# Kernel tuning notes

Hardware: AMD Instinct MI355X
Metric: run time of the kernel (lower is better)

## Reference

```python
import jax, jax.numpy as jnp
import numpy as np

EPS = 1e-5  # PyTorch BatchNorm1d default eps


def _bn_relu(x, gamma, beta):
    # BatchNorm1d in training mode: batch statistics (biased variance), then ReLU
    mu = x.mean(0, keepdims=True)
    var = ((x - mu) ** 2).mean(0, keepdims=True)
    return jax.nn.relu(gamma * (x - mu) / jnp.sqrt(var + EPS) + beta)


def _conv_t(x, w, b, stride, pad):
    # ConvTranspose1d. x: [B,Cin,L]; w: [Cin,Cout,K] (torch layout).
    # Implemented as lhs-dilated conv with flipped kernel; out_len = (L-1)*stride - 2*pad + K
    k = w.shape[-1]
    wk = jnp.transpose(jnp.flip(w, -1), (1, 0, 2))  # [Cout,Cin,K]
    y = jax.lax.conv_general_dilated(
        x, wk, window_strides=(1,), padding=[(k - 1 - pad, k - 1 - pad)],
        lhs_dilation=(stride,), dimension_numbers=("NCH", "OIH", "NCH"))
    return y + b[None, :, None]


def _lorentz(S):
    # Vectorized form of the original triple loop over (batch i, freq j, triad k).
    # S: [B, L], L % 3 == 0. Triads (wp, w0, g) = S[:, k], S[:, k+1], S[:, k+2].
    B, L = S.shape
    w = (0.8 + jnp.arange(L, dtype=S.dtype) / L)[None, :, None]  # [1,L,1] frequency grid
    wp2 = (S[:, 0::3] ** 2)[:, None, :]  # [B,1,K]
    w0 = S[:, 1::3][:, None, :]
    g = S[:, 2::3][:, None, :]
    sub1 = w0 ** 2 - w ** 2                      # [B,L,K]
    denom = sub1 ** 2 + (w * g) ** 2
    e1 = wp2 * sub1 / denom
    e2 = wp2 * w * g / denom
    m = 0.5 * (e1 ** 2 + e2 ** 2)
    n = jnp.sqrt(jnp.maximum(m + 0.5 * e1, 0.0))   # clamp guards sqrt(neg) -> NaN
    kap2 = jnp.maximum(m - 0.5 * e1, 0.0)          # kappa^2 (original squares it anyway)
    dT = 4.0 * n / ((n + 1.0) ** 2 + kap2)
    return dT.sum(-1)  # reduce over triads -> [B,L]


def setup_inputs() -> dict:
    key = jax.random.key(0)
    ks = iter(jax.random.split(key, 40))
    B = 2048
    dims = [8, 1024, 1024, 150]
    d = {"G": jax.random.normal(next(ks), (B, dims[0]), jnp.float32)}
    for i in range(3):
        fi, fo = dims[i], dims[i + 1]
        d[f"w{i+1}"] = jax.random.normal(next(ks), (fo, fi), jnp.float32) / float(np.sqrt(fi))
        d[f"b{i+1}"] = jnp.zeros((fo,), jnp.float32)
        d[f"g{i+1}"] = 1.0 + 0.1 * jax.random.normal(next(ks), (fo,), jnp.float32)
        d[f"be{i+1}"] = 0.1 * jax.random.normal(next(ks), (fo,), jnp.float32)
    specs = [(1, 4, 8), (4, 4, 5), (4, 4, 5)]  # (in_ch, out_ch, kernel)
    for i, (ci, co, k) in enumerate(specs):
        d[f"ct{i+1}_w"] = jax.random.normal(next(ks), (ci, co, k), jnp.float32) / float(np.sqrt(ci * k))
        d[f"ct{i+1}_b"] = 0.01 * jax.random.normal(next(ks), (co,), jnp.float32)
    d["cf_w"] = jax.random.normal(next(ks), (1, 4, 1), jnp.float32) / 2.0
    d["cf_b"] = 0.01 * jax.random.normal(next(ks), (1,), jnp.float32)
    return d


def reference(G, w1, b1, g1, be1, w2, b2, g2, be2, w3, b3, g3, be3,
              ct1_w, ct1_b, ct2_w, ct2_b, ct3_w, ct3_b, cf_w, cf_b):
    out = _bn_relu(G @ w1.T + b1, g1, be1)
    out = _bn_relu(out @ w2.T + b2, g2, be2)
    out = _bn_relu(out @ w3.T + b3, g3, be3)
    out = out[:, None, :]                       # [B,1,150]
    out = _conv_t(out, ct1_w, ct1_b, 2, 3)      # [B,4,300]
    out = _conv_t(out, ct2_w, ct2_b, 1, 2)      # [B,4,300]
    out = _conv_t(out, ct3_w, ct3_b, 1, 2)      # [B,4,300]
    out = jax.lax.conv_general_dilated(
        out, cf_w, (1,), [(0, 0)], dimension_numbers=("NCH", "OIH", "NCH")) + cf_b[None, :, None]
    S = out[:, 0, :]                            # squeeze -> [B,300]
    return _lorentz(S)
```

## Files before the change

kernel.cpp:

```cpp
#include <hip/hip_runtime.h>
#include <hip/hip_bf16.h>

#define EPS 1e-5f

typedef __attribute__((ext_vector_type(8))) short bf16x8;
typedef __attribute__((ext_vector_type(4))) float f32x4;

__device__ __forceinline__ void gload16(const void* g, void* l) {
  __builtin_amdgcn_global_load_lds(
      (const __attribute__((address_space(1))) unsigned int*)g,
      (__attribute__((address_space(3))) unsigned int*)l, 16, 0, 0);
}

__device__ __forceinline__ void split2(float x, short& h, short& l) {
  unsigned u = __float_as_uint(x);
  h = (short)(u >> 16);
  float hf = __uint_as_float(u & 0xFFFF0000u);
  l = (short)(__float_as_uint(x - hf) >> 16);
}
__device__ __forceinline__ void bn_coef(float s, float q, float g, float be,
                                        float& sc, float& sh) {
  float mu = s * (1.f / 2048.f);
  float var = q * (1.f / 2048.f) - mu * mu;
  sc = g * rsqrtf(var + EPS);
  sh = be - mu * sc;
}

__global__ __launch_bounds__(256) void kpre(
    const float* __restrict__ W2, const float* __restrict__ W3,
    ushort* __restrict__ W2thi, ushort* __restrict__ W2tlo,
    ushort* __restrict__ W3hi, ushort* __restrict__ W3lo,
    float4* __restrict__ stv, float4* __restrict__ Y3v,
    float4* __restrict__ outv) {
  int b = blockIdx.x;
  int tid = threadIdx.x;
  if (b < 1024) {
    int c = tid * 4;
    int nt = b >> 6, rr = b & 63;
    int kt = c >> 6, chunk = (c >> 3) & 7, e = c & 7;
    float4 v = *(const float4*)&W2[(size_t)b * 1024 + c];
    float ev[4] = {v.x, v.y, v.z, v.w};
    short hh[4], ll[4];
#pragma unroll
    for (int q = 0; q < 4; ++q) split2(ev[q], hh[q], ll[q]);
    size_t o = ((size_t)(nt * 16 + kt) << 12) + rr * 64 + ((chunk ^ (rr & 7)) << 3) + e;
    *(ushort4*)&W2thi[o] = make_ushort4((ushort)hh[0], (ushort)hh[1],
                                        (ushort)hh[2], (ushort)hh[3]);
    *(ushort4*)&W2tlo[o] = make_ushort4((ushort)ll[0], (ushort)ll[1],
                                        (ushort)ll[2], (ushort)ll[3]);
  } else if (b < 1029) {
    int idx = (b - 1024) * 256 + tid;
    if (idx < 1112) stv[idx] = make_float4(0.f, 0.f, 0.f, 0.f);
  } else if (b < 1189) {
    int n = b - 1029;
    int c = tid * 4;
    float4 v = make_float4(0.f, 0.f, 0.f, 0.f);
    if (n < 150) v = *(const float4*)&W3[(size_t)n * 1024 + c];
    float e[4] = {v.x, v.y, v.z, v.w};
    short hh[4], ll[4];
#pragma unroll
    for (int q = 0; q < 4; ++q) split2(e[q], hh[q], ll[q]);
    *(ushort4*)&W3hi[(size_t)n * 1024 + c] =
        make_ushort4((ushort)hh[0], (ushort)hh[1], (ushort)hh[2], (ushort)hh[3]);
    *(ushort4*)&W3lo[(size_t)n * 1024 + c] =
        make_ushort4((ushort)ll[0], (ushort)ll[1], (ushort)ll[2], (ushort)ll[3]);
  } else if (b < 1489) {
    Y3v[(b - 1189) * 256 + tid] = make_float4(0.f, 0.f, 0.f, 0.f);
  } else {
    outv[(b - 1489) * 256 + tid] = make_float4(0.f, 0.f, 0.f, 0.f);
  }
}

__global__ __launch_bounds__(256) void k1s(const float* __restrict__ G,
                                           const float* __restrict__ W1,
                                           float* __restrict__ sA1,
                                           float* __restrict__ qA1) {
  int r0 = blockIdx.x * 8;
  int c = threadIdx.x * 4;
  float w[4][8];
#pragma unroll
  for (int q = 0; q < 4; ++q)
#pragma unroll
    for (int k = 0; k < 8; ++k) w[q][k] = W1[(c + q) * 8 + k];
  float s[4] = {}, ss[4] = {};
  for (int r = 0; r < 8; ++r) {
    const float4 g0 = *(const float4*)&G[(size_t)(r0 + r) * 8];
    const float4 g1 = *(const float4*)&G[(size_t)(r0 + r) * 8 + 4];
    float gr[8] = {g0.x, g0.y, g0.z, g0.w, g1.x, g1.y, g1.z, g1.w};
#pragma unroll
    for (int q = 0; q < 4; ++q) {
      float acc = 0.f;
#pragma unroll
      for (int k = 0; k < 8; ++k) acc += gr[k] * w[q][k];
      s[q] += acc;
      ss[q] += acc * acc;
    }
  }
#pragma unroll
  for (int q = 0; q < 4; ++q) {
    atomicAdd(&sA1[c + q], s[q]);
    atomicAdd(&qA1[c + q], ss[q]);
  }
}

__global__ __launch_bounds__(256) void k1c(
    const float* __restrict__ G, const float* __restrict__ W1,
    const float* __restrict__ sA1, const float* __restrict__ qA1,
    const float* __restrict__ g1, const float* __restrict__ be1,
    ushort* __restrict__ X1thi, ushort* __restrict__ X1tlo) {
  int r0 = blockIdx.x * 8;
  int c = threadIdx.x * 4;
  float w[4][8];
#pragma unroll
  for (int q = 0; q < 4; ++q)
#pragma unroll
    for (int k = 0; k < 8; ++k) w[q][k] = W1[(c + q) * 8 + k];
  float sc[4], sh[4];
#pragma unroll
  for (int q = 0; q < 4; ++q)
    bn_coef(sA1[c + q], qA1[c + q], g1[c + q], be1[c + q], sc[q], sh[q]);
  int kt = c >> 6, chunk = (c >> 3) & 7, e = c & 7;
  for (int r = 0; r < 8; ++r) {
    int b = r0 + r;
    const float4 g0 = *(const float4*)&G[(size_t)b * 8];
    const float4 g1v = *(const float4*)&G[(size_t)b * 8 + 4];
    float gr[8] = {g0.x, g0.y, g0.z, g0.w, g1v.x, g1v.y, g1v.z, g1v.w};
    short hs[4], ls[4];
#pragma unroll
    for (int q = 0; q < 4; ++q) {
      float acc = 0.f;
#pragma unroll
      for (int k = 0; k < 8; ++k) acc += gr[k] * w[q][k];
      float x = fmaxf(0.f, acc * sc[q] + sh[q]);
      split2(x, hs[q], ls[q]);
    }
    int mt = b >> 7, rr = b & 127;
    size_t o = ((size_t)(mt * 16 + kt) << 13) + rr * 64 + ((chunk ^ (rr & 7)) << 3) + e;
    *(ushort4*)&X1thi[o] = make_ushort4((ushort)hs[0], (ushort)hs[1],
                                        (ushort)hs[2], (ushort)hs[3]);
    *(ushort4*)&X1tlo[o] = make_ushort4((ushort)ls[0], (ushort)ls[1],
                                        (ushort)ls[2], (ushort)ls[3]);
  }
}

__global__ __launch_bounds__(512) void k2_mfma(
    const ushort* __restrict__ X1thi, const ushort* __restrict__ X1tlo,
    const ushort* __restrict__ W2thi, const ushort* __restrict__ W2tlo,
    float* __restrict__ Y2, float* __restrict__ sA2, float* __restrict__ qA2) {
  __shared__ short lAhi[128 * 64], lAlo[128 * 64];
  __shared__ short lBhi[64 * 64], lBlo[64 * 64];
  int id = blockIdx.x;
  int xcd = id & 7, slot = id >> 3;
  int g = slot >> 4, wi = slot & 15;
  int bx = (xcd & 3) * 4 + (wi & 3);
  int by = ((xcd >> 2) * 2 + g) * 4 + (wi >> 2);
  int b0 = bx * 128, j0 = by * 64;
  int tid = threadIdx.x;
  int lane = tid & 63, wave = tid >> 6;
  int wm = wave >> 1, wn = wave & 1;
  int woff = wave * 1024 + lane * 16;
  int loff = wave * 1024;
  f32x4 acc[2][2] = {};
  for (int kt = 0; kt < 16; ++kt) {
    const char* ga = (const char*)(X1thi + ((size_t)(bx * 16 + kt) << 13));
    const char* gl = (const char*)(X1tlo + ((size_t)(bx * 16 + kt) << 13));
    const char* gb = (const char*)(W2thi + ((size_t)(by * 16 + kt) << 12));
    const char* gc = (const char*)(W2tlo + ((size_t)(by * 16 + kt) << 12));
    gload16(ga + woff, (char*)lAhi + loff);
    gload16(ga + woff + 8192, (char*)lAhi + loff + 8192);
    gload16(gl + woff, (char*)lAlo + loff);
    gload16(gl + woff + 8192, (char*)lAlo + loff + 8192);
    gload16(gb + woff, (char*)lBhi + loff);
    gload16(gc + woff, (char*)lBlo + loff);
    __syncthreads();
#pragma unroll
    for (int kk = 0; kk < 2; ++kk) {
      int ch = kk * 4 + (lane >> 4);
      bf16x8 ah[2], al[2], bh[2], bl[2];
#pragma unroll
      for (int mi = 0; mi < 2; ++mi) {
        int rr = wm * 32 + mi * 16 + (lane & 15);
        int ad = rr * 64 + ((ch ^ (rr & 7)) << 3);
        ah[mi] = *(const bf16x8*)&lAhi[ad];
        al[mi] = *(const bf16x8*)&lAlo[ad];
      }
#pragma unroll
      for (int ni = 0; ni < 2; ++ni) {
        int rr = wn * 32 + ni * 16 + (lane & 15);
        int bd = rr * 64 + ((ch ^ (rr & 7)) << 3);
        bh[ni] = *(const bf16x8*)&lBhi[bd];
        bl[ni] = *(const bf16x8*)&lBlo[bd];
      }
#pragma unroll
      for (int mi = 0; mi < 2; ++mi)
#pragma unroll
        for (int ni = 0; ni < 2; ++ni) {
          acc[mi][ni] = __builtin_amdgcn_mfma_f32_16x16x32_bf16(
              ah[mi], bh[ni], acc[mi][ni], 0, 0, 0);
          acc[mi][ni] = __builtin_amdgcn_mfma_f32_16x16x32_bf16(
              al[mi], bh[ni], acc[mi][ni], 0, 0, 0);
          acc[mi][ni] = __builtin_amdgcn_mfma_f32_16x16x32_bf16(
              ah[mi], bl[ni], acc[mi][ni], 0, 0, 0);
        }
    }
    __syncthreads();
  }
#pragma unroll
  for (int mi = 0; mi < 2; ++mi)
#pragma unroll
    for (int ni = 0; ni < 2; ++ni) {
      int col = j0 + wn * 32 + ni * 16 + (lane & 15);
#pragma unroll
      for (int r = 0; r < 4; ++r) {
        int row = b0 + wm * 32 + mi * 16 + (lane >> 4) * 4 + r;
        Y2[(size_t)row * 1024 + col] = acc[mi][ni][r];
      }
    }
#pragma unroll
  for (int ni = 0; ni < 2; ++ni) {
    float s = 0.f, q = 0.f;
#pragma unroll
    for (int mi = 0; mi < 2; ++mi)
#pragma unroll
      for (int r = 0; r < 4; ++r) {
        float v = acc[mi][ni][r];
        s += v;
        q += v * v;
      }
    s += __shfl_xor(s, 16);
    q += __shfl_xor(q, 16);
    s += __shfl_xor(s, 32);
    q += __shfl_xor(q, 32);
    if ((lane >> 4) == 0) {
      int col = j0 + wn * 32 + ni * 16 + lane;
      atomicAdd(&sA2[col], s);
      atomicAdd(&qA2[col], q);
    }
  }
}

__global__ __launch_bounds__(256) void k4_mfma(
    const float* __restrict__ Y2, const float* __restrict__ sA2,
    const float* __restrict__ qA2, const float* __restrict__ g2,
    const float* __restrict__ be2, const ushort* __restrict__ W3hi,
    const ushort* __restrict__ W3lo, float* __restrict__ Y3) {
  __shared__ short lAhi[32 * 64], lAlo[32 * 64];
  int b0 = blockIdx.x * 32;
  int kb = blockIdx.y * 128;
  int tid = threadIdx.x;
  int lane = tid & 63, wave = tid >> 6;
  int wm = wave & 1, wn = wave >> 1;
  f32x4 acc[5] = {};
  int srow = tid >> 3, sch = tid & 7;
  for (int k0 = 0; k0 < 128; k0 += 64) {
    int kg = kb + k0 + sch * 8;
    const float* src = &Y2[(size_t)(b0 + srow) * 1024 + kg];
    float4 f0 = *(const float4*)src;
    float4 f1 = *(const float4*)(src + 4);
    float4 sv0 = *(const float4*)&sA2[kg];
    float4 sv1 = *(const float4*)&sA2[kg + 4];
    float4 qv0 = *(const float4*)&qA2[kg];
    float4 qv1 = *(const float4*)&qA2[kg + 4];
    float4 gv0 = *(const float4*)&g2[kg];
    float4 gv1 = *(const float4*)&g2[kg + 4];
    float4 bv0 = *(const float4*)&be2[kg];
    float4 bv1 = *(const float4*)&be2[kg + 4];
    float e[8] = {f0.x, f0.y, f0.z, f0.w, f1.x, f1.y, f1.z, f1.w};
    float sv[8] = {sv0.x, sv0.y, sv0.z, sv0.w, sv1.x, sv1.y, sv1.z, sv1.w};
    float qv[8] = {qv0.x, qv0.y, qv0.z, qv0.w, qv1.x, qv1.y, qv1.z, qv1.w};
    float gv[8] = {gv0.x, gv0.y, gv0.z, gv0.w, gv1.x, gv1.y, gv1.z, gv1.w};
    float bev[8] = {bv0.x, bv0.y, bv0.z, bv0.w, bv1.x, bv1.y, bv1.z, bv1.w};
    bf16x8 hh, ll;
#pragma unroll
    for (int q = 0; q < 8; ++q) {
      float sc, sh;
      bn_coef(sv[q], qv[q], gv[q], bev[q], sc, sh);
      float x = fmaxf(0.f, fmaf(e[q], sc, sh));
      short h, l;
      split2(x, h, l);
      hh[q] = h;
      ll[q] = l;
    }
    if (k0) __syncthreads();
    int d = srow * 64 + ((sch ^ (srow & 7)) << 3);
    *(bf16x8*)&lAhi[d] = hh;
    *(bf16x8*)&lAlo[d] = ll;
    __syncthreads();
#pragma unroll
    for (int kk = 0; kk < 2; ++kk) {
      int r = wm * 16 + (lane & 15);
      int ch = kk * 4 + (lane >> 4);
      int ad = r * 64 + ((ch ^ (r & 7)) << 3);
      bf16x8 ah = *(const bf16x8*)&lAhi[ad];
      bf16x8 al = *(const bf16x8*)&lAlo[ad];
#pragma unroll
      for (int ni = 0; ni < 5; ++ni) {
        int col = wn * 80 + ni * 16 + (lane & 15);
        size_t wo = (size_t)col * 1024 + kb + k0 + kk * 32 + (lane >> 4) * 8;
        bf16x8 bh = *(const bf16x8*)&W3hi[wo];
        bf16x8 bl = *(const bf16x8*)&W3lo[wo];
        acc[ni] = __builtin_amdgcn_mfma_f32_16x16x32_bf16(ah, bh, acc[ni], 0, 0, 0);
        acc[ni] = __builtin_amdgcn_mfma_f32_16x16x32_bf16(al, bh, acc[ni], 0, 0, 0);
        acc[ni] = __builtin_amdgcn_mfma_f32_16x16x32_bf16(ah, bl, acc[ni], 0, 0, 0);
      }
    }
  }
#pragma unroll
  for (int ni = 0; ni < 5; ++ni) {
    int col = wn * 80 + ni * 16 + (lane & 15);
    if (col < 150) {
#pragma unroll
      for (int r = 0; r < 4; ++r) {
        int row = b0 + wm * 16 + (lane >> 4) * 4 + r;
        atomicAdd(&Y3[(size_t)row * 150 + col], acc[ni][r]);
      }
    }
  }
}

__global__ __launch_bounds__(256) void k5s(const float* __restrict__ Y3,
                                           float* __restrict__ sA3,
                                           float* __restrict__ qA3) {
  int r0 = blockIdx.x * 8;
  int j = threadIdx.x;
  if (j >= 150) return;
  float s = 0.f, q = 0.f;
  for (int r = 0; r < 8; ++r) {
    float v = Y3[(size_t)(r0 + r) * 150 + j];
    s += v;
    q += v * v;
  }
  atomicAdd(&sA3[j], s);
  atomicAdd(&qA3[j], q);
}

__global__ __launch_bounds__(256) void k6a(
    const float* __restrict__ Y3, const float* __restrict__ sA3,
    const float* __restrict__ qA3, const float* __restrict__ g3,
    const float* __restrict__ be3, const float* __restrict__ ct1_w,
    const float* __restrict__ ct1_b, const float* __restrict__ ct2_w,
    const float* __restrict__ ct2_b, const float* __restrict__ ct3_w,
    const float* __restrict__ ct3_b, const float* __restrict__ cf_w,
    const float* __restrict__ cf_b, float* __restrict__ Spre) {
  __shared__ float wt1[32], wb1[4], wt2L[80], wb2L[4], w3fL[20];
  __shared__ float Cc[36], cfb2C[1], cfbraw[1];
  __shared__ float h0p[4][160];
  __shared__ float hA[4][4][312];
  __shared__ float Srow[4][304];
  int tid = threadIdx.x;
  if (tid < 32) wt1[tid] = ct1_w[tid];
  else if (tid < 36) wb1[tid - 32] = ct1_b[tid - 32];
  else if (tid < 116) wt2L[tid - 36] = ct2_w[tid - 36];
  else if (tid < 120) wb2L[tid - 116] = ct2_b[tid - 116];
  else if (tid < 140) {
    int i = (tid - 120) / 5, j = (tid - 120) % 5;
    float s = 0.f;
#pragma unroll
    for (int p = 0; p < 4; ++p) s += cf_w[p] * ct3_w[(i * 4 + p) * 5 + j];
    w3fL[tid - 120] = s;
  } else if (tid == 140) {
    float s = cf_b[0];
#pragma unroll
    for (int p = 0; p < 4; ++p) s += cf_w[p] * ct3_b[p];
    cfbraw[0] = s;
  }
  int w = tid >> 6;
  int lane = tid & 63;
  int r = blockIdx.x * 4 + w;
  for (int i = lane; i < 160; i += 64) {
    int k = i - 2;
    float v = 0.f;
    if (k >= 0 && k < 150) {
      float sc, sh;
      bn_coef(sA3[k], qA3[k], g3[k], be3[k], sc, sh);
      v = fmaxf(0.f, Y3[(size_t)r * 150 + k] * sc + sh);
    }
    h0p[w][i] = v;
  }
  if (lane < 12) {
    int z = (lane < 4) ? lane : (300 + lane);
#pragma unroll
    for (int o = 0; o < 4; ++o) hA[w][o][z] = 0.f;
  }
  __syncthreads();
  if (tid < 36) {
    int i = tid / 9, u = tid % 9;
    float s = 0.f;
#pragma unroll
    for (int o = 0; o < 4; ++o) {
      int j2lo = (u > 4) ? (u - 4) : 0;
      int j2hi = (u < 4) ? u : 4;
      for (int j2 = j2lo; j2 <= j2hi; ++j2)
        s += wt2L[(i * 4 + o) * 5 + (u - j2)] * w3fL[o * 5 + j2];
    }
    Cc[tid] = s;
  } else if (tid == 36) {
    float s = cfbraw[0];
#pragma unroll
    for (int o = 0; o < 4; ++o) {
      float t = 0.f;
#pragma unroll
      for (int j2 = 0; j2 < 5; ++j2) t += w3fL[o * 5 + j2];
      s += wb2L[o] * t;
    }
    cfb2C[0] = s;
  }
  __syncthreads();
  for (int t = lane; t < 300; t += 64) {
    int p1 = (t + 3) & 1;
    int base = (t + 3 - p1) >> 1;
    float x0 = h0p[w][2 + base];
    float x1 = h0p[w][1 + base];
    float x2 = h0p[w][base];
    float x3 = h0p[w][base - 1];
#pragma unroll
    for (int o = 0; o < 4; ++o) {
      float acc = wb1[o];
      acc += wt1[o * 8 + p1] * x0;
      acc += wt1[o * 8 + p1 + 2] * x1;
      acc += wt1[o * 8 + p1 + 4] * x2;
      acc += wt1[o * 8 + p1 + 6] * x3;
      hA[w][o][4 + t] = acc;
    }
  }
  __syncthreads();
  for (int t = lane; t < 300; t += 64) {
    float acc = cfb2C[0];
#pragma unroll
    for (int i = 0; i < 4; ++i)
#pragma unroll
      for (int u = 0; u < 9; ++u) acc += Cc[i * 9 + u] * hA[w][i][t + 8 - u];
    if (t < 2) {
      for (int j2 = t + 3; j2 <= 4; ++j2) {
        int tp_ = t + 2 - j2;
        float corr = 0.f;
        for (int o = 0; o < 4; ++o) {
          float hb = wb2L[o];
          for (int i2 = 0; i2 < 4; ++i2)
            for (int j1 = 0; j1 < 5; ++j1)
              hb += wt2L[(i2 * 4 + o) * 5 + j1] * hA[w][i2][6 + tp_ - j1];
          corr += w3fL[o * 5 + j2] * hb;
        }
        acc -= corr;
      }
    }
    if (t > 297) {
      for (int j2 = 0; j2 <= t - 298; ++j2) {
        int tp_ = t + 2 - j2;
        float corr = 0.f;
        for (int o = 0; o < 4; ++o) {
          float hb = wb2L[o];
          for (int i2 = 0; i2 < 4; ++i2)
            for (int j1 = 0; j1 < 5; ++j1)
              hb += wt2L[(i2 * 4 + o) * 5 + j1] * hA[w][i2][6 + tp_ - j1];
          corr += w3fL[o * 5 + j2] * hb;
        }
        acc -= corr;
      }
    }
    Srow[w][t] = acc;
  }
  __syncthreads();
  for (int cc = lane; cc < 100; cc += 64) {
    float s0 = Srow[w][3 * cc], s1 = Srow[w][3 * cc + 1], s2 = Srow[w][3 * cc + 2];
    float P = s0 * s0, s1s = s1 * s1, s2s = s2 * s2;
    float halfP = 0.5f * P;
    float4 q0, q1;
    q0.x = s2s - 2.f * s1s;
    q0.y = s1s * s1s;
    q0.z = halfP * (P + s1s);
    q0.w = halfP;
    q1.x = halfP * (P - s1s);
    q1.y = 0.f;
    q1.z = 0.f;
    q1.w = 0.f;
    size_t o = ((size_t)r * 100 + cc) * 8;
    *(float4*)&Spre[o] = q0;
    *(float4*)&Spre[o + 4] = q1;
  }
}

__global__ __launch_bounds__(320) void k6b(const float* __restrict__ Spre,
                                           float* __restrict__ out) {
  int b = blockIdx.x;
  int l = threadIdx.x;
  float wl = 0.8f + (float)l * (1.0f / 300.0f);
  float x = wl * wl;
  float xn = -x;
  float acc = 0.f;
  const float4* pp = (const float4*)(Spre + (size_t)b * 800) + blockIdx.y * 50;
#pragma unroll 5
  for (int cc = 0; cc < 25; ++cc) {
    float4 q0 = pp[2 * cc];
    float4 q1 = pp[2 * cc + 1];
    float D = fmaf(x, x + q0.x, q0.y);
    float t1 = fmaxf(fmaf(q0.w, xn, q0.z), 0.f);
    float t2 = fmaxf(fmaf(q0.w, x, q1.x), 0.f);
    float R = __builtin_amdgcn_sqrtf(t1 * D);
    float sum = (t1 + D) + fmaf(2.f, R, t2);
    acc = fmaf(R, __builtin_amdgcn_rcpf(sum), acc);
  }
  if (l < 300) atomicAdd(&out[(size_t)b * 300 + l], 4.0f * acc);
}

extern "C" void kernel_launch(void* const* d_in, const int* in_sizes, int n_in,
                              void* d_out, int out_size, void* d_ws,
                              size_t ws_size, hipStream_t stream) {
  const float* G = (const float*)d_in[0];
  const float* w1 = (const float*)d_in[1];
  const float* g1 = (const float*)d_in[3];
  const float* be1 = (const float*)d_in[4];
  const float* w2 = (const float*)d_in[5];
  const float* g2 = (const float*)d_in[7];
  const float* be2 = (const float*)d_in[8];
  const float* w3 = (const float*)d_in[9];
  const float* g3 = (const float*)d_in[11];
  const float* be3 = (const float*)d_in[12];
  const float* ct1_w = (const float*)d_in[13];
  const float* ct1_b = (const float*)d_in[14];
  const float* ct2_w = (const float*)d_in[15];
  const float* ct2_b = (const float*)d_in[16];
  const float* ct3_w = (const float*)d_in[17];
  const float* ct3_b = (const float*)d_in[18];
  const float* cf_w = (const float*)d_in[19];
  const float* cf_b = (const float*)d_in[20];
  float* out = (float*)d_out;

  float* ws = (float*)d_ws;
  float* Y2 = ws;
  float* Spre = ws;
  ushort* X1thi = (ushort*)(ws + 2097152);
  ushort* X1tlo = (ushort*)(ws + 3145728);
  float* sA1 = ws + 4194304;
  float* qA1 = sA1 + 1024;
  float* sA2 = sA1 + 2048;
  float* qA2 = sA1 + 3072;
  float* sA3 = sA1 + 4096;
  float* qA3 = sA1 + 4288;
  ushort* W2thi = (ushort*)(ws + 4198752);
  ushort* W2tlo = (ushort*)(ws + 4723040);
  ushort* W3hi = (ushort*)(ws + 5247328);
  ushort* W3lo = (ushort*)(ws + 5329248);
  float* Y3 = ws + 5411168;

  kpre<<<2089, 256, 0, stream>>>(w2, w3, W2thi, W2tlo, W3hi, W3lo,
                                 (float4*)sA1, (float4*)Y3, (float4*)out);
  k1s<<<256, 256, 0, stream>>>(G, w1, sA1, qA1);
  k1c<<<256, 256, 0, stream>>>(G, w1, sA1, qA1, g1, be1, X1thi, X1tlo);
  k2_mfma<<<256, 512, 0, stream>>>(X1thi, X1tlo, W2thi, W2tlo, Y2, sA2, qA2);
  k4_mfma<<<dim3(64, 8), 256, 0, stream>>>(Y2, sA2, qA2, g2, be2, W3hi, W3lo, Y3);
  k5s<<<256, 256, 0, stream>>>(Y3, sA3, qA3);
  k6a<<<512, 256, 0, stream>>>(Y3, sA3, qA3, g3, be3, ct1_w, ct1_b, ct2_w,
                               ct2_b, ct3_w, ct3_b, cf_w, cf_b, Spre);
  k6b<<<dim3(2048, 4), 320, 0, stream>>>(Spre, out);
}
```

Baseline: 139.6 us.

## Replace float atomics with deterministic partial buffers and separate reduction kernels

Every atomicAdd reduction is replaced with writes to per-partition buffers followed by dedicated reduction kernels. This covers the BN statistics for layers 1–3, the split-K accumulation into Y3, and the split Lorentz sum into the output. Dropping the atomics also removes the zero-initialisation work from kpre, and BN2 scale/shift are precomputed once instead of being recomputed per element in k4. The aim is to cut atomic contention and make results deterministic. The cost is three extra kernel launches, extra global traffic for the partial buffers, and reused workspace regions that must not overlap while live.

```diff
diff --git a/kernel.cpp b/kernel.cpp
--- a/kernel.cpp
+++ b/kernel.cpp
@@ -29,9 +29,7 @@
 __global__ __launch_bounds__(256) void kpre(
     const float* __restrict__ W2, const float* __restrict__ W3,
     ushort* __restrict__ W2thi, ushort* __restrict__ W2tlo,
-    ushort* __restrict__ W3hi, ushort* __restrict__ W3lo,
-    float4* __restrict__ stv, float4* __restrict__ Y3v,
-    float4* __restrict__ outv) {
+    ushort* __restrict__ W3hi, ushort* __restrict__ W3lo) {
   int b = blockIdx.x;
   int tid = threadIdx.x;
   if (b < 1024) {
@@ -48,11 +46,8 @@
                                         (ushort)hh[2], (ushort)hh[3]);
     *(ushort4*)&W2tlo[o] = make_ushort4((ushort)ll[0], (ushort)ll[1],
                                         (ushort)ll[2], (ushort)ll[3]);
-  } else if (b < 1029) {
-    int idx = (b - 1024) * 256 + tid;
-    if (idx < 1112) stv[idx] = make_float4(0.f, 0.f, 0.f, 0.f);
-  } else if (b < 1189) {
-    int n = b - 1029;
+  } else {
+    int n = b - 1024;
     int c = tid * 4;
     float4 v = make_float4(0.f, 0.f, 0.f, 0.f);
     if (n < 150) v = *(const float4*)&W3[(size_t)n * 1024 + c];
@@ -64,10 +59,6 @@
         make_ushort4((ushort)hh[0], (ushort)hh[1], (ushort)hh[2], (ushort)hh[3]);
     *(ushort4*)&W3lo[(size_t)n * 1024 + c] =
         make_ushort4((ushort)ll[0], (ushort)ll[1], (ushort)ll[2], (ushort)ll[3]);
-  } else if (b < 1489) {
-    Y3v[(b - 1189) * 256 + tid] = make_float4(0.f, 0.f, 0.f, 0.f);
-  } else {
-    outv[(b - 1489) * 256 + tid] = make_float4(0.f, 0.f, 0.f, 0.f);
   }
 }
 
@@ -75,17 +66,19 @@
                                            const float* __restrict__ W1,
                                            float* __restrict__ sA1,
                                            float* __restrict__ qA1) {
-  int r0 = blockIdx.x * 8;
-  int c = threadIdx.x * 4;
+  __shared__ float rs[4][256], rq[4][256];
+  int c0 = blockIdx.x * 4;
+  int tid = threadIdx.x;
   float w[4][8];
 #pragma unroll
   for (int q = 0; q < 4; ++q)
 #pragma unroll
-    for (int k = 0; k < 8; ++k) w[q][k] = W1[(c + q) * 8 + k];
+    for (int k = 0; k < 8; ++k) w[q][k] = W1[(c0 + q) * 8 + k];
   float s[4] = {}, ss[4] = {};
-  for (int r = 0; r < 8; ++r) {
-    const float4 g0 = *(const float4*)&G[(size_t)(r0 + r) * 8];
-    const float4 g1 = *(const float4*)&G[(size_t)(r0 + r) * 8 + 4];
+  for (int i = 0; i < 8; ++i) {
+    int r = tid * 8 + i;
+    const float4 g0 = *(const float4*)&G[(size_t)r * 8];
+    const float4 g1 = *(const float4*)&G[(size_t)r * 8 + 4];
     float gr[8] = {g0.x, g0.y, g0.z, g0.w, g1.x, g1.y, g1.z, g1.w};
 #pragma unroll
     for (int q = 0; q < 4; ++q) {
@@ -98,8 +91,23 @@
   }
 #pragma unroll
   for (int q = 0; q < 4; ++q) {
-    atomicAdd(&sA1[c + q], s[q]);
-    atomicAdd(&qA1[c + q], ss[q]);
+    rs[q][tid] = s[q];
+    rq[q][tid] = ss[q];
+  }
+  __syncthreads();
+  for (int off = 128; off > 0; off >>= 1) {
+    if (tid < off) {
+#pragma unroll
+      for (int q = 0; q < 4; ++q) {
+        rs[q][tid] += rs[q][tid + off];
+        rq[q][tid] += rq[q][tid + off];
+      }
+    }
+    __syncthreads();
+  }
+  if (tid < 4) {
+    sA1[c0 + tid] = rs[tid][0];
+    qA1[c0 + tid] = rq[tid][0];
   }
 }
 
@@ -146,7 +154,7 @@
 __global__ __launch_bounds__(512) void k2_mfma(
     const ushort* __restrict__ X1thi, const ushort* __restrict__ X1tlo,
     const ushort* __restrict__ W2thi, const ushort* __restrict__ W2tlo,
-    float* __restrict__ Y2, float* __restrict__ sA2, float* __restrict__ qA2) {
+    float* __restrict__ Y2, float* __restrict__ s2p, float* __restrict__ q2p) {
   __shared__ short lAhi[128 * 64], lAlo[128 * 64];
   __shared__ short lBhi[64 * 64], lBlo[64 * 64];
   int id = blockIdx.x;
@@ -233,20 +241,44 @@
     q += __shfl_xor(q, 32);
     if ((lane >> 4) == 0) {
       int col = j0 + wn * 32 + ni * 16 + lane;
-      atomicAdd(&sA2[col], s);
-      atomicAdd(&qA2[col], q);
-    }
+      int p = bx * 4 + wm;
+      s2p[p * 1024 + col] = s;
+      q2p[p * 1024 + col] = q;
+    }
+  }
+}
+
+__global__ __launch_bounds__(64) void kc2(const float* __restrict__ s2p,
+                                          const float* __restrict__ q2p,
+                                          const float* __restrict__ g2,
+                                          const float* __restrict__ be2,
+                                          float* __restrict__ scale2,
+                                          float* __restrict__ shift2) {
+  int j = blockIdx.x;
+  int t = threadIdx.x;
+  float s = s2p[t * 1024 + j];
+  float q = q2p[t * 1024 + j];
+#pragma unroll
+  for (int off = 32; off > 0; off >>= 1) {
+    s += __shfl_xor(s, off);
+    q += __shfl_xor(q, off);
+  }
+  if (t == 0) {
+    float sc, sh;
+    bn_coef(s, q, g2[j], be2[j], sc, sh);
+    scale2[j] = sc;
+    shift2[j] = sh;
   }
 }
 
 __global__ __launch_bounds__(256) void k4_mfma(
-    const float* __restrict__ Y2, const float* __restrict__ sA2,
-    const float* __restrict__ qA2, const float* __restrict__ g2,
-    const float* __restrict__ be2, const ushort* __restrict__ W3hi,
-    const ushort* __restrict__ W3lo, float* __restrict__ Y3) {
+    const float* __restrict__ Y2, const float* __restrict__ scale2,
+    const float* __restrict__ shift2, const ushort* __restrict__ W3hi,
+    const ushort* __restrict__ W3lo, float* __restrict__ P) {
   __shared__ short lAhi[32 * 64], lAlo[32 * 64];
   int b0 = blockIdx.x * 32;
-  int kb = blockIdx.y * 128;
+  int kz = blockIdx.y;
+  int kb = kz * 128;
   int tid = threadIdx.x;
   int lane = tid & 63, wave = tid >> 6;
   int wm = wave & 1, wn = wave >> 1;
@@ -257,25 +289,17 @@
     const float* src = &Y2[(size_t)(b0 + srow) * 1024 + kg];
     float4 f0 = *(const float4*)src;
     float4 f1 = *(const float4*)(src + 4);
-    float4 sv0 = *(const float4*)&sA2[kg];
-    float4 sv1 = *(const float4*)&sA2[kg + 4];
-    float4 qv0 = *(const float4*)&qA2[kg];
-    float4 qv1 = *(const float4*)&qA2[kg + 4];
-    float4 gv0 = *(const float4*)&g2[kg];
-    float4 gv1 = *(const float4*)&g2[kg + 4];
-    float4 bv0 = *(const float4*)&be2[kg];
-    float4 bv1 = *(const float4*)&be2[kg + 4];
+    float4 c0 = *(const float4*)&scale2[kg];
+    float4 c1 = *(const float4*)&scale2[kg + 4];
+    float4 s0 = *(const float4*)&shift2[kg];
+    float4 s1 = *(const float4*)&shift2[kg + 4];
     float e[8] = {f0.x, f0.y, f0.z, f0.w, f1.x, f1.y, f1.z, f1.w};
-    float sv[8] = {sv0.x, sv0.y, sv0.z, sv0.w, sv1.x, sv1.y, sv1.z, sv1.w};
-    float qv[8] = {qv0.x, qv0.y, qv0.z, qv0.w, qv1.x, qv1.y, qv1.z, qv1.w};
-    float gv[8] = {gv0.x, gv0.y, gv0.z, gv0.w, gv1.x, gv1.y, gv1.z, gv1.w};
-    float bev[8] = {bv0.x, bv0.y, bv0.z, bv0.w, bv1.x, bv1.y, bv1.z, bv1.w};
+    float cs[8] = {c0.x, c0.y, c0.z, c0.w, c1.x, c1.y, c1.z, c1.w};
+    float sh[8] = {s0.x, s0.y, s0.z, s0.w, s1.x, s1.y, s1.z, s1.w};
     bf16x8 hh, ll;
 #pragma unroll
     for (int q = 0; q < 8; ++q) {
-      float sc, sh;
-      bn_coef(sv[q], qv[q], gv[q], bev[q], sc, sh);
-      float x = fmaxf(0.f, fmaf(e[q], sc, sh));
+      float x = fmaxf(0.f, fmaf(e[q], cs[q], sh[q]));
       short h, l;
       split2(x, h, l);
       hh[q] = h;
@@ -312,26 +336,54 @@
 #pragma unroll
       for (int r = 0; r < 4; ++r) {
         int row = b0 + wm * 16 + (lane >> 4) * 4 + r;
-        atomicAdd(&Y3[(size_t)row * 150 + col], acc[ni][r]);
-      }
-    }
-  }
-}
-
-__global__ __launch_bounds__(256) void k5s(const float* __restrict__ Y3,
-                                           float* __restrict__ sA3,
-                                           float* __restrict__ qA3) {
+        P[(size_t)kz * 307200 + (size_t)row * 150 + col] = acc[ni][r];
+      }
+    }
+  }
+}
+
+__global__ __launch_bounds__(192) void k5a(const float* __restrict__ P,
+                                           float* __restrict__ Y3,
+                                           float* __restrict__ p3s,
+                                           float* __restrict__ p3q) {
   int r0 = blockIdx.x * 8;
   int j = threadIdx.x;
   if (j >= 150) return;
   float s = 0.f, q = 0.f;
   for (int r = 0; r < 8; ++r) {
-    float v = Y3[(size_t)(r0 + r) * 150 + j];
+    size_t base = (size_t)(r0 + r) * 150 + j;
+    float v = P[base];
+#pragma unroll
+    for (int kz = 1; kz < 8; ++kz) v += P[(size_t)kz * 307200 + base];
+    Y3[base] = v;
     s += v;
     q += v * v;
   }
-  atomicAdd(&sA3[j], s);
-  atomicAdd(&qA3[j], q);
+  p3s[blockIdx.x * 160 + j] = s;
+  p3q[blockIdx.x * 160 + j] = q;
+}
+
+__global__ __launch_bounds__(256) void k5b(const float* __restrict__ p3s,
+                                           const float* __restrict__ p3q,
+                                           float* __restrict__ sA3,
+                                           float* __restrict__ qA3) {
+  __shared__ float rs[256], rq[256];
+  int j = blockIdx.x;
+  int t = threadIdx.x;
+  rs[t] = p3s[t * 160 + j];
+  rq[t] = p3q[t * 160 + j];
+  __syncthreads();
+  for (int off = 128; off > 0; off >>= 1) {
+    if (t < off) {
+      rs[t] += rs[t + off];
+      rq[t] += rq[t + off];
+    }
+    __syncthreads();
+  }
+  if (t == 0) {
+    sA3[j] = rs[0];
+    qA3[j] = rq[0];
+  }
 }
 
 __global__ __launch_bounds__(256) void k6a(
@@ -481,14 +533,15 @@
 }
 
 __global__ __launch_bounds__(320) void k6b(const float* __restrict__ Spre,
-                                           float* __restrict__ out) {
+                                           float* __restrict__ op) {
   int b = blockIdx.x;
+  int y = blockIdx.y;
   int l = threadIdx.x;
   float wl = 0.8f + (float)l * (1.0f / 300.0f);
   float x = wl * wl;
   float xn = -x;
   float acc = 0.f;
-  const float4* pp = (const float4*)(Spre + (size_t)b * 800) + blockIdx.y * 50;
+  const float4* pp = (const float4*)(Spre + (size_t)b * 800) + y * 50;
 #pragma unroll 5
   for (int cc = 0; cc < 25; ++cc) {
     float4 q0 = pp[2 * cc];
@@ -500,7 +553,22 @@
     float sum = (t1 + D) + fmaf(2.f, R, t2);
     acc = fmaf(R, __builtin_amdgcn_rcpf(sum), acc);
   }
-  if (l < 300) atomicAdd(&out[(size_t)b * 300 + l], 4.0f * acc);
+  if (l < 300) op[(size_t)y * 614400 + (size_t)b * 300 + l] = 4.0f * acc;
+}
+
+__global__ __launch_bounds__(256) void k6c(const float4* __restrict__ op4,
+                                           float4* __restrict__ out4) {
+  int i = blockIdx.x * 256 + threadIdx.x;
+  float4 a = op4[i];
+  float4 b = op4[i + 153600];
+  float4 c = op4[i + 307200];
+  float4 d = op4[i + 460800];
+  float4 r;
+  r.x = ((a.x + b.x) + c.x) + d.x;
+  r.y = ((a.y + b.y) + c.y) + d.y;
+  r.z = ((a.z + b.z) + c.z) + d.z;
+  r.w = ((a.w + b.w) + c.w) + d.w;
+  out4[i] = r;
 }
 
 extern "C" void kernel_launch(void* const* d_in, const int* in_sizes, int n_in,
@@ -531,26 +599,34 @@
   float* Spre = ws;
   ushort* X1thi = (ushort*)(ws + 2097152);
   ushort* X1tlo = (ushort*)(ws + 3145728);
-  float* sA1 = ws + 4194304;
-  float* qA1 = sA1 + 1024;
-  float* sA2 = sA1 + 2048;
-  float* qA2 = sA1 + 3072;
-  float* sA3 = sA1 + 4096;
-  float* qA3 = sA1 + 4288;
-  ushort* W2thi = (ushort*)(ws + 4198752);
-  ushort* W2tlo = (ushort*)(ws + 4723040);
-  ushort* W3hi = (ushort*)(ws + 5247328);
-  ushort* W3lo = (ushort*)(ws + 5329248);
-  float* Y3 = ws + 5411168;
-
-  kpre<<<2089, 256, 0, stream>>>(w2, w3, W2thi, W2tlo, W3hi, W3lo,
-                                 (float4*)sA1, (float4*)Y3, (float4*)out);
+  ushort* W2thi = (ushort*)(ws + 4194304);
+  ushort* W2tlo = (ushort*)(ws + 4718592);
+  float* P = ws + 2097152;
+  float* op = ws + 2097152;
+  ushort* W3hi = (ushort*)(ws + 5242880);
+  ushort* W3lo = (ushort*)(ws + 5324800);
+  float* s2p = ws + 5406720;
+  float* q2p = ws + 5472256;
+  float* sA1 = ws + 5537792;
+  float* qA1 = ws + 5538816;
+  float* Y3 = ws + 5406720;
+  float* p3s = ws + 5713920;
+  float* p3q = ws + 5754880;
+  float* sA3 = ws + 5795840;
+  float* qA3 = ws + 5796000;
+  float* scale2 = ws + 5796160;
+  float* shift2 = ws + 5797184;
+
+  kpre<<<1184, 256, 0, stream>>>(w2, w3, W2thi, W2tlo, W3hi, W3lo);
   k1s<<<256, 256, 0, stream>>>(G, w1, sA1, qA1);
   k1c<<<256, 256, 0, stream>>>(G, w1, sA1, qA1, g1, be1, X1thi, X1tlo);
-  k2_mfma<<<256, 512, 0, stream>>>(X1thi, X1tlo, W2thi, W2tlo, Y2, sA2, qA2);
-  k4_mfma<<<dim3(64, 8), 256, 0, stream>>>(Y2, sA2, qA2, g2, be2, W3hi, W3lo, Y3);
-  k5s<<<256, 256, 0, stream>>>(Y3, sA3, qA3);
+  k2_mfma<<<256, 512, 0, stream>>>(X1thi, X1tlo, W2thi, W2tlo, Y2, s2p, q2p);
+  kc2<<<1024, 64, 0, stream>>>(s2p, q2p, g2, be2, scale2, shift2);
+  k4_mfma<<<dim3(64, 8), 256, 0, stream>>>(Y2, scale2, shift2, W3hi, W3lo, P);
+  k5a<<<256, 192, 0, stream>>>(P, Y3, p3s, p3q);
+  k5b<<<150, 256, 0, stream>>>(p3s, p3q, sA3, qA3);
   k6a<<<512, 256, 0, stream>>>(Y3, sA3, qA3, g3, be3, ct1_w, ct1_b, ct2_w,
                                ct2_b, ct3_w, ct3_b, cf_w, cf_b, Spre);
-  k6b<<<dim3(2048, 4), 320, 0, stream>>>(Spre, out);
-}
+  k6b<<<dim3(2048, 4), 320, 0, stream>>>(Spre, op);
+  k6c<<<600, 256, 0, stream>>>((const float4*)op, (float4*)out);
+}
```

After: 116.1 us. -16.8%, faster.
